# Kernel optimization log

Measured on AMD Instinct MI355X. Metric: run time of the kernel, lower is better.

Reference implementation:

```python
import jax, jax.numpy as jnp
import numpy as np
from math import sqrt

ALPHA = 1.0
EPS = 1e-8


def setup_inputs() -> dict:
    key = jax.random.key(0)
    k1, k2, k3 = jax.random.split(key, 3)
    B, L, S, H, E = 4, 2048, 2048, 8, 64
    queries = jax.random.normal(k1, (B, L, H, E), dtype=jnp.float32)
    keys = jax.random.normal(k2, (B, S, H, E), dtype=jnp.float32)
    values = jax.random.normal(k3, (B, S, H, E), dtype=jnp.float32)
    return {"queries": queries, "keys": keys, "values": values}


def reference(queries, keys, values):
    B, L, H, E = queries.shape
    scale = 1.0 / sqrt(E)
    # [B,H,L,S] dot-product scores
    dot_product = jnp.einsum('blhe,bshe->bhls', queries, keys)
    # squared norms: [B,H,L,1] and [B,H,1,S]
    queries_norm2 = jnp.sum(queries * queries, axis=-1).transpose(0, 2, 1)[..., None]
    keys_norm2 = jnp.sum(keys * keys, axis=-1).transpose(0, 2, 1)[..., None, :]
    # wedge (exterior product) norm: |q|^2|k|^2 - (q.k)^2, clamped at 0
    wedge_norm2 = jax.nn.relu(queries_norm2 * keys_norm2 - dot_product * dot_product)
    wedge_norm = jnp.sqrt(wedge_norm2 + EPS)
    scores = ((1.0 - ALPHA) * dot_product + ALPHA * wedge_norm) * scale
    A = jax.nn.softmax(scores, axis=-1)  # dropout p=0 (eval)
    V = jnp.einsum('bhls,bshd->blhd', A, values)
    return V, jnp.mean(jnp.abs(scores))
```

## Files before the change

### kernel.cpp

```cpp
#include <hip/hip_runtime.h>
#include <hip/hip_bf16.h>


#define B_ 4
#define L_ 2048
#define S_ 2048
#define H_ 8
#define E_ 64
#define EPS_ 1e-8f
#define SC2_ 0.18033688011112042f
#define LN2_ 0.6931471805599453f
#define LDP 72
#define ROWSTR (H_ * E_)

#define K_OFF 0
#define V_OFF 8388608
#define KN_OFF 16777216
#define SS_OFF 17039360
#define WS_NEED 17039364

typedef __attribute__((ext_vector_type(8))) short bf16x8;
typedef __attribute__((ext_vector_type(4))) short bf16x4v;
typedef __attribute__((ext_vector_type(4))) float f32x4;

static __device__ __forceinline__ short f2bf_rne(float x) {
  union { float f; unsigned u; } v; v.f = x;
  unsigned r = (v.u + 0x7FFF + ((v.u >> 16) & 1)) >> 16;
  return (short)(unsigned short)r;
}
static __device__ __forceinline__ float bf2f(short h) {
  union { unsigned u; float f; } v; v.u = ((unsigned)(unsigned short)h) << 16;
  return v.f;
}
static __device__ __forceinline__ float fast_sqrt(float x) {
  float r; asm("v_sqrt_f32 %0, %1" : "=v"(r) : "v"(x)); return r;
}
static __device__ __forceinline__ float fast_exp2(float x) {
  float r; asm("v_exp_f32 %0, %1" : "=v"(r) : "v"(x)); return r;
}
static __device__ __forceinline__ void gload16(const void* g, void* l) {
  __builtin_amdgcn_global_load_lds((const __attribute__((address_space(1))) void*)g,
                                   (__attribute__((address_space(3))) void*)l, 16, 0, 0);
}

__global__ void prep_k(const float* __restrict__ K, short* __restrict__ Kg,
                       float* __restrict__ kn2g) {
  const int tid = threadIdx.x;
  const int bidx = blockIdx.x;
  const int st = bidx & 31;
  const int bh = bidx >> 5;
  const int b = bh >> 3, h = bh & 7;
  const size_t src_base = (size_t)b * (L_ * ROWSTR) + (size_t)(st * 64) * ROWSTR + (size_t)h * E_;
  short* dst = Kg + (size_t)bidx * 4096;

  const int s = tid >> 2;
  float part = 0.f;
#pragma unroll
  for (int q = 0; q < 2; ++q) {
    const int ci = 2 * tid + q;
    const int ch = ci & 7;
    const int esrc = (ch ^ (s & 7)) * 8;
    const float* sp = K + src_base + (size_t)s * ROWSTR + esrc;
    const float4 a = *reinterpret_cast<const float4*>(sp);
    const float4 c4 = *reinterpret_cast<const float4*>(sp + 4);
    part += a.x*a.x + a.y*a.y + a.z*a.z + a.w*a.w
          + c4.x*c4.x + c4.y*c4.y + c4.z*c4.z + c4.w*c4.w;
    bf16x8 o;
    o[0]=f2bf_rne(a.x); o[1]=f2bf_rne(a.y); o[2]=f2bf_rne(a.z); o[3]=f2bf_rne(a.w);
    o[4]=f2bf_rne(c4.x); o[5]=f2bf_rne(c4.y); o[6]=f2bf_rne(c4.z); o[7]=f2bf_rne(c4.w);
    *reinterpret_cast<bf16x8*>(dst + s * 64 + ch * 8) = o;
  }
  part += __shfl_xor(part, 1);
  part += __shfl_xor(part, 2);
  if ((tid & 3) == 0) kn2g[(size_t)bidx * 64 + s] = part;
}

__global__ void prep_v(const float* __restrict__ V, short* __restrict__ Vg) {
  __shared__ __align__(16) short TT[64][72];
  const int tid = threadIdx.x;
  const int bidx = blockIdx.x;
  const int st = bidx & 31;
  const int bh = bidx >> 5;
  const int b = bh >> 3, h = bh & 7;
  const size_t src_base = (size_t)b * (L_ * ROWSTR) + (size_t)(st * 64) * ROWSTR + (size_t)h * E_;
  short* dst = Vg + (size_t)bidx * 4096;

  const int s = tid >> 2;
  const int e0 = (tid & 3) * 16;
  const float* sp = V + src_base + (size_t)s * ROWSTR + e0;
#pragma unroll
  for (int q = 0; q < 4; ++q) {
    const float4 a = *reinterpret_cast<const float4*>(sp + q * 4);
    TT[e0 + q*4 + 0][s] = f2bf_rne(a.x);
    TT[e0 + q*4 + 1][s] = f2bf_rne(a.y);
    TT[e0 + q*4 + 2][s] = f2bf_rne(a.z);
    TT[e0 + q*4 + 3][s] = f2bf_rne(a.w);
  }
  __syncthreads();
  const int e = s;
#pragma unroll
  for (int q = 0; q < 2; ++q) {
    const int ci = 2 * tid + q;
    const int ch = ci & 7;
    const int ssrc = (ch ^ (e & 7)) * 8;
    const bf16x8 v = *reinterpret_cast<const bf16x8*>(&TT[e][ssrc]);
    *reinterpret_cast<bf16x8*>(dst + e * 64 + ch * 8) = v;
  }
}

__launch_bounds__(256, 2)
__global__ void geom_attn(const float* __restrict__ Q,
                          const short* __restrict__ Kg,
                          const short* __restrict__ Vg,
                          const float* __restrict__ kn2g,
                          float* __restrict__ out,
                          float* __restrict__ ssum_g) {
  __shared__ __align__(16) short Kl[2][4096];
  __shared__ __align__(16) short Vl[2][4096];
  __shared__ __align__(16) short Plds[4][16 * LDP];

  const int tid = threadIdx.x;
  const int lane = tid & 63;
  const int w = tid >> 6;
  const int g = lane >> 4;
  const int c = lane & 15;
  const int cx = c & 7;

  const int vbk = ((blockIdx.x & 7) << 7) + (blockIdx.x >> 3);
  const int qt = vbk & 31;
  const int bh = vbk >> 5;
  const int b = bh >> 3, h = bh & 7;
  const int q0 = qt * 64;

  const size_t qbase = (size_t)b * (L_ * ROWSTR) + (size_t)h * E_;

  bf16x8 qa[2];
  float qn2row[4];
  {
    const int qrow = q0 + w * 16 + c;
    const float* qp = Q + qbase + (size_t)qrow * ROWSTR;
    float qs = 0.f;
#pragma unroll
    for (int ch = 0; ch < 2; ++ch) {
      const float4 a = *reinterpret_cast<const float4*>(qp + ch * 32 + g * 8);
      const float4 b4 = *reinterpret_cast<const float4*>(qp + ch * 32 + g * 8 + 4);
      qa[ch][0]=f2bf_rne(a.x); qa[ch][1]=f2bf_rne(a.y); qa[ch][2]=f2bf_rne(a.z); qa[ch][3]=f2bf_rne(a.w);
      qa[ch][4]=f2bf_rne(b4.x); qa[ch][5]=f2bf_rne(b4.y); qa[ch][6]=f2bf_rne(b4.z); qa[ch][7]=f2bf_rne(b4.w);
      qs += a.x*a.x + a.y*a.y + a.z*a.z + a.w*a.w
          + b4.x*b4.x + b4.y*b4.y + b4.z*b4.z + b4.w*b4.w;
    }
    qs += __shfl_xor(qs, 16);
    qs += __shfl_xor(qs, 32);
#pragma unroll
    for (int i = 0; i < 4; ++i) qn2row[i] = __shfl(qs, g * 4 + i);
  }

  float lsum[4] = {0.f, 0.f, 0.f, 0.f};
  f32x4 o[4];
#pragma unroll
  for (int dt = 0; dt < 4; ++dt) o[dt] = (f32x4){0.f, 0.f, 0.f, 0.f};
  float ssum = 0.f;

  const char* Ksrc = (const char*)(Kg + (size_t)(bh * 32) * 4096);
  const char* Vsrc = (const char*)(Vg + (size_t)(bh * 32) * 4096);
  const float* knb = kn2g + (size_t)(bh * 32) * 64;

  const int wb = w * 2048;

  gload16(Ksrc + wb + lane * 16,        (char*)&Kl[0][0] + wb);
  gload16(Ksrc + wb + 1024 + lane * 16, (char*)&Kl[0][0] + wb + 1024);
  gload16(Vsrc + wb + lane * 16,        (char*)&Vl[0][0] + wb);
  gload16(Vsrc + wb + 1024 + lane * 16, (char*)&Vl[0][0] + wb + 1024);

  for (int kt = 0; kt < 32; ++kt) {
    const int cb = kt & 1;
    __syncthreads();

    if (kt + 1 < 32) {
      const char* ks2 = Ksrc + (size_t)(kt + 1) * 8192;
      const char* vs2 = Vsrc + (size_t)(kt + 1) * 8192;
      gload16(ks2 + wb + lane * 16,        (char*)&Kl[cb ^ 1][0] + wb);
      gload16(ks2 + wb + 1024 + lane * 16, (char*)&Kl[cb ^ 1][0] + wb + 1024);
      gload16(vs2 + wb + lane * 16,        (char*)&Vl[cb ^ 1][0] + wb);
      gload16(vs2 + wb + 1024 + lane * 16, (char*)&Vl[cb ^ 1][0] + wb + 1024);
    }

    float kn_r[4];
#pragma unroll
    for (int sub = 0; sub < 4; ++sub) kn_r[sub] = knb[kt * 64 + sub * 16 + c];

#pragma unroll
    for (int sub = 0; sub < 4; ++sub) {
      const int s = sub * 16 + c;
      f32x4 acc = (f32x4){0.f, 0.f, 0.f, 0.f};
#pragma unroll
      for (int ch = 0; ch < 2; ++ch) {
        const int idx = s * 64 + (((ch * 4 + g) ^ cx) << 3);
        const bf16x8 bh8 = *reinterpret_cast<const bf16x8*>(&Kl[cb][idx]);
        acc = __builtin_amdgcn_mfma_f32_16x16x32_bf16(qa[ch], bh8, acc, 0, 0, 0);
      }
#pragma unroll
      for (int i = 0; i < 4; ++i) {
        const float dot = acc[i];
        const float w2 = fmaxf(fmaf(-dot, dot, qn2row[i] * kn_r[sub]), EPS_);
        const float s2 = SC2_ * fast_sqrt(w2);
        ssum += s2;
        const float p = fast_exp2(s2);
        union { float f; unsigned u; } pu; pu.f = p;
        union { unsigned u; float f; } pt; pt.u = pu.u & 0xffff0000u;
        lsum[i] += pt.f;
        Plds[w][(g * 4 + i) * LDP + s] = (short)(unsigned short)(pu.u >> 16);
      }
    }

#pragma unroll
    for (int ks = 0; ks < 2; ++ks) {
      const bf16x8 pa = *reinterpret_cast<const bf16x8*>(&Plds[w][c * LDP + ks * 32 + g * 8]);
#pragma unroll
      for (int dt = 0; dt < 4; ++dt) {
        const int er = dt * 16 + c;
        const int idx = er * 64 + (((ks * 4 + g) ^ cx) << 3);
        const bf16x8 vb8 = *reinterpret_cast<const bf16x8*>(&Vl[cb][idx]);
        o[dt] = __builtin_amdgcn_mfma_f32_16x16x32_bf16(pa, vb8, o[dt], 0, 0, 0);
      }
    }
  }

#pragma unroll
  for (int m = 1; m < 16; m <<= 1)
#pragma unroll
    for (int i = 0; i < 4; ++i) lsum[i] += __shfl_xor(lsum[i], m);

#pragma unroll
  for (int i = 0; i < 4; ++i) {
    const float inv = 1.0f / lsum[i];
    const int qrow = q0 + w * 16 + g * 4 + i;
    float* op = out + (size_t)b * (L_ * ROWSTR) + (size_t)qrow * ROWSTR + (size_t)h * E_;
#pragma unroll
    for (int dt = 0; dt < 4; ++dt)
      op[dt * 16 + c] = o[dt][i] * inv;
  }

#pragma unroll
  for (int m = 1; m < 64; m <<= 1) ssum += __shfl_xor(ssum, m);
  if (lane == 0) atomicAdd(ssum_g, ssum);
}

__global__ void geom_fin(const float* __restrict__ ws, float* __restrict__ out) {
  out[(size_t)B_ * L_ * H_ * E_] = ws[0] * (LN2_ / 134217728.0f);
}

__launch_bounds__(256, 2)
__global__ void geom_attn_v1(const float* __restrict__ Q, const float* __restrict__ K,
                             const float* __restrict__ V, float* __restrict__ out,
                             float* __restrict__ score_sum) {
  __shared__ __align__(16) short Khi[64 * LDP];
  __shared__ __align__(16) short Klo[64 * LDP];
  __shared__ __align__(16) short Vt[64 * LDP];
  __shared__ __align__(16) short Plds[4][16 * LDP];
  __shared__ float kn2[64];
  __shared__ float qn2[64];

  const int tid = threadIdx.x;
  const int lane = tid & 63;
  const int w = tid >> 6;
  const int g = lane >> 4;
  const int c = lane & 15;
  const int bidx = blockIdx.x;
  const int qt = bidx & 31;
  const int h = (bidx >> 5) & 7;
  const int b = bidx >> 8;
  const int q0 = qt * 64;
  const size_t bh_base = (size_t)b * L_ * ROWSTR + (size_t)h * E_;

  bf16x8 qhi[2], qlo[2];
  {
    const int qrow = q0 + w * 16 + c;
    const float* qp = Q + bh_base + (size_t)qrow * ROWSTR;
    float qs = 0.f;
#pragma unroll
    for (int ch = 0; ch < 2; ++ch) {
      const float4 a = *reinterpret_cast<const float4*>(qp + ch * 32 + g * 8);
      const float4 bq = *reinterpret_cast<const float4*>(qp + ch * 32 + g * 8 + 4);
      const float xs[8] = {a.x,a.y,a.z,a.w,bq.x,bq.y,bq.z,bq.w};
#pragma unroll
      for (int j = 0; j < 8; ++j) {
        const float x = xs[j];
        qs += x * x;
        const short hs = f2bf_rne(x);
        qhi[ch][j] = hs;
        qlo[ch][j] = f2bf_rne(x - bf2f(hs));
      }
    }
    qs += __shfl_xor(qs, 16);
    qs += __shfl_xor(qs, 32);
    if (lane < 16) qn2[w * 16 + c] = qs;
  }
  __syncthreads();
  float qn2row[4];
#pragma unroll
  for (int i = 0; i < 4; ++i) qn2row[i] = qn2[w * 16 + g * 4 + i];

  float m_i[4] = {0,0,0,0}, lsum[4] = {0,0,0,0};
  f32x4 o[4];
#pragma unroll
  for (int dt = 0; dt < 4; ++dt) o[dt] = (f32x4){0,0,0,0};
  float ssum = 0.f;

  for (int kt = 0; kt < S_ / 64; ++kt) {
    __syncthreads();
    {
      const int r0 = tid >> 4, c4 = tid & 15;
      const size_t kbase = bh_base + (size_t)(kt * 64) * ROWSTR + c4 * 4;
      float part[4];
#pragma unroll
      for (int i = 0; i < 4; ++i) {
        const int r = r0 + 16 * i;
        const float4 kv = *reinterpret_cast<const float4*>(K + kbase + (size_t)r * ROWSTR);
        part[i] = kv.x*kv.x + kv.y*kv.y + kv.z*kv.z + kv.w*kv.w;
        const short h0 = f2bf_rne(kv.x), h1 = f2bf_rne(kv.y), h2 = f2bf_rne(kv.z), h3 = f2bf_rne(kv.w);
        bf16x4v hv = {h0, h1, h2, h3};
        *reinterpret_cast<bf16x4v*>(&Khi[r * LDP + c4 * 4]) = hv;
        bf16x4v lv = {f2bf_rne(kv.x - bf2f(h0)), f2bf_rne(kv.y - bf2f(h1)),
                      f2bf_rne(kv.z - bf2f(h2)), f2bf_rne(kv.w - bf2f(h3))};
        *reinterpret_cast<bf16x4v*>(&Klo[r * LDP + c4 * 4]) = lv;
        const float4 vv = *reinterpret_cast<const float4*>(V + kbase + (size_t)r * ROWSTR);
        Vt[(c4 * 4 + 0) * LDP + r] = f2bf_rne(vv.x);
        Vt[(c4 * 4 + 1) * LDP + r] = f2bf_rne(vv.y);
        Vt[(c4 * 4 + 2) * LDP + r] = f2bf_rne(vv.z);
        Vt[(c4 * 4 + 3) * LDP + r] = f2bf_rne(vv.w);
      }
#pragma unroll
      for (int m = 1; m < 16; m <<= 1)
#pragma unroll
        for (int i = 0; i < 4; ++i) part[i] += __shfl_xor(part[i], m);
      if (c4 < 4) kn2[r0 + 16 * c4] = part[c4];
    }
    __syncthreads();

    float sv[4][4];
    float tm[4] = {0,0,0,0};
#pragma unroll
    for (int sub = 0; sub < 4; ++sub) {
      const int s = sub * 16 + c;
      f32x4 acc = (f32x4){0,0,0,0};
#pragma unroll
      for (int ch = 0; ch < 2; ++ch) {
        const int e = ch * 32 + g * 8;
        const bf16x8 bh8 = *reinterpret_cast<const bf16x8*>(&Khi[s * LDP + e]);
        const bf16x8 bl8 = *reinterpret_cast<const bf16x8*>(&Klo[s * LDP + e]);
        acc = __builtin_amdgcn_mfma_f32_16x16x32_bf16(qhi[ch], bh8, acc, 0, 0, 0);
        acc = __builtin_amdgcn_mfma_f32_16x16x32_bf16(qlo[ch], bh8, acc, 0, 0, 0);
        acc = __builtin_amdgcn_mfma_f32_16x16x32_bf16(qhi[ch], bl8, acc, 0, 0, 0);
      }
      const float kn = kn2[s];
#pragma unroll
      for (int i = 0; i < 4; ++i) {
        const float dot = acc[i];
        float w2 = fmaxf(qn2row[i] * kn - dot * dot, 0.f) + EPS_;
        const float sc = 0.125f * sqrtf(w2);
        sv[sub][i] = sc;
        tm[i] = fmaxf(tm[i], sc);
        ssum += sc;
      }
    }
#pragma unroll
    for (int m = 1; m < 16; m <<= 1)
#pragma unroll
      for (int i = 0; i < 4; ++i) tm[i] = fmaxf(tm[i], __shfl_xor(tm[i], m));
    float r_[4];
#pragma unroll
    for (int i = 0; i < 4; ++i) {
      const float mn = fmaxf(m_i[i], tm[i]);
      r_[i] = __expf(m_i[i] - mn);
      m_i[i] = mn;
      lsum[i] *= r_[i];
    }
#pragma unroll
    for (int dt = 0; dt < 4; ++dt)
#pragma unroll
      for (int i = 0; i < 4; ++i) o[dt][i] *= r_[i];
#pragma unroll
    for (int sub = 0; sub < 4; ++sub) {
      const int s = sub * 16 + c;
#pragma unroll
      for (int i = 0; i < 4; ++i) {
        const float p = __expf(sv[sub][i] - m_i[i]);
        lsum[i] += p;
        Plds[w][(g * 4 + i) * LDP + s] = f2bf_rne(p);
      }
    }
    __syncthreads();
#pragma unroll
    for (int ks = 0; ks < 2; ++ks) {
      const bf16x8 pa = *reinterpret_cast<const bf16x8*>(&Plds[w][c * LDP + ks * 32 + g * 8]);
#pragma unroll
      for (int dt = 0; dt < 4; ++dt) {
        const bf16x8 vb8 = *reinterpret_cast<const bf16x8*>(&Vt[(dt * 16 + c) * LDP + ks * 32 + g * 8]);
        o[dt] = __builtin_amdgcn_mfma_f32_16x16x32_bf16(pa, vb8, o[dt], 0, 0, 0);
      }
    }
  }
#pragma unroll
  for (int m = 1; m < 16; m <<= 1)
#pragma unroll
    for (int i = 0; i < 4; ++i) lsum[i] += __shfl_xor(lsum[i], m);
#pragma unroll
  for (int i = 0; i < 4; ++i) {
    const float inv = 1.0f / lsum[i];
    const int qrow = q0 + w * 16 + g * 4 + i;
    float* op = out + (size_t)b * L_ * ROWSTR + (size_t)qrow * ROWSTR + (size_t)h * E_;
#pragma unroll
    for (int dt = 0; dt < 4; ++dt) op[dt * 16 + c] = o[dt][i] * inv;
  }
#pragma unroll
  for (int m = 1; m < 64; m <<= 1) ssum += __shfl_xor(ssum, m);
  if (lane == 0) atomicAdd(score_sum, ssum);
}

__global__ void geom_fin_v1(const float* __restrict__ ws, float* __restrict__ out) {
  out[(size_t)B_ * L_ * H_ * E_] = ws[0] * (1.0f / 134217728.0f);
}

extern "C" void kernel_launch(void* const* d_in, const int* in_sizes, int n_in,
                              void* d_out, int out_size, void* d_ws, size_t ws_size,
                              hipStream_t stream) {
  const float* Q = (const float*)d_in[0];
  const float* K = (const float*)d_in[1];
  const float* V = (const float*)d_in[2];
  float* out = (float*)d_out;

  if (ws_size >= (size_t)WS_NEED) {
    short* Kg = (short*)((char*)d_ws + K_OFF);
    short* Vg = (short*)((char*)d_ws + V_OFF);
    float* kn2g = (float*)((char*)d_ws + KN_OFF);
    float* ss = (float*)((char*)d_ws + SS_OFF);
    hipMemsetAsync(ss, 0, sizeof(float), stream);
    prep_k<<<dim3(1024), dim3(256), 0, stream>>>(K, Kg, kn2g);
    prep_v<<<dim3(1024), dim3(256), 0, stream>>>(V, Vg);
    geom_attn<<<dim3(1024), dim3(256), 0, stream>>>(Q, Kg, Vg, kn2g, out, ss);
    geom_fin<<<dim3(1), dim3(1), 0, stream>>>(ss, out);
  } else {
    float* ss = (float*)d_ws;
    hipMemsetAsync(ss, 0, sizeof(float), stream);
    geom_attn_v1<<<dim3(1024), dim3(256), 0, stream>>>(Q, K, V, out, ss);
    geom_fin_v1<<<dim3(1), dim3(1), 0, stream>>>(ss, out);
  }
}
```

Baseline: 209.5 us.

## Merge K/V prep kernels, single-buffer V, raise occupancy, prefetch key norms

Fuses the separate K and V preparation kernels into one launch and switches to packed bf16 conversion intrinsics. In the attention kernel, V is now single-buffered: it is loaded at the start of each tile and waited on with a manual vmcnt plus barrier before the PV MFMAs. This frees LDS so launch bounds can rise from 2 to 4 blocks per CU. Key norms are also prefetched one tile ahead. The cost is that V load latency is exposed inside each iteration instead of being hidden by double-buffering, and there is an extra barrier per tile.

```diff
diff --git a/kernel.cpp b/kernel.cpp
--- a/kernel.cpp
+++ b/kernel.cpp
@@ -23,6 +23,13 @@
 typedef __attribute__((ext_vector_type(4))) short bf16x4v;
 typedef __attribute__((ext_vector_type(4))) float f32x4;
 
+union bfr8 { bf16x8 v; unsigned u[4]; };
+
+static __device__ __forceinline__ unsigned pk2(float lo, float hi) {
+  union { __hip_bfloat162 h2; unsigned u; } cv;
+  cv.h2 = __float22bfloat162_rn(float2{lo, hi});
+  return cv.u;
+}
 static __device__ __forceinline__ short f2bf_rne(float x) {
   union { float f; unsigned u; } v; v.f = x;
   unsigned r = (v.u + 0x7FFF + ((v.u >> 16) & 1)) >> 16;
@@ -43,72 +50,77 @@
                                    (__attribute__((address_space(3))) void*)l, 16, 0, 0);
 }
 
-__global__ void prep_k(const float* __restrict__ K, short* __restrict__ Kg,
-                       float* __restrict__ kn2g) {
+__global__ void prep_kv(const float* __restrict__ K, const float* __restrict__ V,
+                        short* __restrict__ Kg, short* __restrict__ Vg,
+                        float* __restrict__ kn2g) {
+  __shared__ __align__(16) short TT[64 * 80];
   const int tid = threadIdx.x;
-  const int bidx = blockIdx.x;
+  const int raw = blockIdx.x;
+  const bool isK = raw < 1024;
+  const int bidx = isK ? raw : raw - 1024;
   const int st = bidx & 31;
   const int bh = bidx >> 5;
   const int b = bh >> 3, h = bh & 7;
   const size_t src_base = (size_t)b * (L_ * ROWSTR) + (size_t)(st * 64) * ROWSTR + (size_t)h * E_;
-  short* dst = Kg + (size_t)bidx * 4096;
-
-  const int s = tid >> 2;
-  float part = 0.f;
-#pragma unroll
-  for (int q = 0; q < 2; ++q) {
-    const int ci = 2 * tid + q;
-    const int ch = ci & 7;
-    const int esrc = (ch ^ (s & 7)) * 8;
-    const float* sp = K + src_base + (size_t)s * ROWSTR + esrc;
-    const float4 a = *reinterpret_cast<const float4*>(sp);
-    const float4 c4 = *reinterpret_cast<const float4*>(sp + 4);
-    part += a.x*a.x + a.y*a.y + a.z*a.z + a.w*a.w
-          + c4.x*c4.x + c4.y*c4.y + c4.z*c4.z + c4.w*c4.w;
-    bf16x8 o;
-    o[0]=f2bf_rne(a.x); o[1]=f2bf_rne(a.y); o[2]=f2bf_rne(a.z); o[3]=f2bf_rne(a.w);
-    o[4]=f2bf_rne(c4.x); o[5]=f2bf_rne(c4.y); o[6]=f2bf_rne(c4.z); o[7]=f2bf_rne(c4.w);
-    *reinterpret_cast<bf16x8*>(dst + s * 64 + ch * 8) = o;
-  }
-  part += __shfl_xor(part, 1);
-  part += __shfl_xor(part, 2);
-  if ((tid & 3) == 0) kn2g[(size_t)bidx * 64 + s] = part;
-}
-
-__global__ void prep_v(const float* __restrict__ V, short* __restrict__ Vg) {
-  __shared__ __align__(16) short TT[64][72];
-  const int tid = threadIdx.x;
-  const int bidx = blockIdx.x;
-  const int st = bidx & 31;
-  const int bh = bidx >> 5;
-  const int b = bh >> 3, h = bh & 7;
-  const size_t src_base = (size_t)b * (L_ * ROWSTR) + (size_t)(st * 64) * ROWSTR + (size_t)h * E_;
-  short* dst = Vg + (size_t)bidx * 4096;
-
-  const int s = tid >> 2;
-  const int e0 = (tid & 3) * 16;
-  const float* sp = V + src_base + (size_t)s * ROWSTR + e0;
-#pragma unroll
-  for (int q = 0; q < 4; ++q) {
-    const float4 a = *reinterpret_cast<const float4*>(sp + q * 4);
-    TT[e0 + q*4 + 0][s] = f2bf_rne(a.x);
-    TT[e0 + q*4 + 1][s] = f2bf_rne(a.y);
-    TT[e0 + q*4 + 2][s] = f2bf_rne(a.z);
-    TT[e0 + q*4 + 3][s] = f2bf_rne(a.w);
-  }
-  __syncthreads();
-  const int e = s;
-#pragma unroll
-  for (int q = 0; q < 2; ++q) {
-    const int ci = 2 * tid + q;
-    const int ch = ci & 7;
-    const int ssrc = (ch ^ (e & 7)) * 8;
-    const bf16x8 v = *reinterpret_cast<const bf16x8*>(&TT[e][ssrc]);
-    *reinterpret_cast<bf16x8*>(dst + e * 64 + ch * 8) = v;
-  }
-}
-
-__launch_bounds__(256, 2)
+
+  if (isK) {
+    short* dst = Kg + (size_t)bidx * 4096;
+    const int s = tid >> 2;
+    float part = 0.f;
+#pragma unroll
+    for (int q = 0; q < 2; ++q) {
+      const int ch = (2 * tid + q) & 7;
+      const int esrc = (ch ^ (s & 7)) * 8;
+      const float* sp = K + src_base + (size_t)s * ROWSTR + esrc;
+      const float4 a = *reinterpret_cast<const float4*>(sp);
+      const float4 c4 = *reinterpret_cast<const float4*>(sp + 4);
+      part += a.x*a.x + a.y*a.y + a.z*a.z + a.w*a.w
+            + c4.x*c4.x + c4.y*c4.y + c4.z*c4.z + c4.w*c4.w;
+      bfr8 o;
+      o.u[0] = pk2(a.x, a.y);  o.u[1] = pk2(a.z, a.w);
+      o.u[2] = pk2(c4.x, c4.y); o.u[3] = pk2(c4.z, c4.w);
+      *reinterpret_cast<bf16x8*>(dst + s * 64 + ch * 8) = o.v;
+    }
+    part += __shfl_xor(part, 1);
+    part += __shfl_xor(part, 2);
+    if ((tid & 3) == 0) kn2g[(size_t)bidx * 64 + s] = part;
+  } else {
+    short* dst = Vg + (size_t)bidx * 4096;
+    {
+      const int s = tid >> 2;
+      const int e0 = (tid & 3) * 16;
+      const float* sp = V + src_base + (size_t)s * ROWSTR + e0;
+      const float4 a0 = *reinterpret_cast<const float4*>(sp);
+      const float4 a1 = *reinterpret_cast<const float4*>(sp + 4);
+      const float4 a2 = *reinterpret_cast<const float4*>(sp + 8);
+      const float4 a3 = *reinterpret_cast<const float4*>(sp + 12);
+      bfr8 t0, t1;
+      t0.u[0] = pk2(a0.x, a0.y); t0.u[1] = pk2(a0.z, a0.w);
+      t0.u[2] = pk2(a1.x, a1.y); t0.u[3] = pk2(a1.z, a1.w);
+      t1.u[0] = pk2(a2.x, a2.y); t1.u[1] = pk2(a2.z, a2.w);
+      t1.u[2] = pk2(a3.x, a3.y); t1.u[3] = pk2(a3.z, a3.w);
+      *reinterpret_cast<bf16x8*>(&TT[s * 80 + e0]) = t0.v;
+      *reinterpret_cast<bf16x8*>(&TT[s * 80 + e0 + 8]) = t1.v;
+    }
+    __syncthreads();
+    const int e = tid >> 2;
+#pragma unroll
+    for (int q = 0; q < 2; ++q) {
+      const int ch = (2 * tid + q) & 7;
+      const int s0 = (ch ^ (e & 7)) * 8;
+      bfr8 o;
+#pragma unroll
+      for (int j = 0; j < 4; ++j) {
+        const unsigned lo = (unsigned short)TT[(s0 + 2 * j) * 80 + e];
+        const unsigned hi = (unsigned short)TT[(s0 + 2 * j + 1) * 80 + e];
+        o.u[j] = lo | (hi << 16);
+      }
+      *reinterpret_cast<bf16x8*>(dst + e * 64 + ch * 8) = o.v;
+    }
+  }
+}
+
+__launch_bounds__(256, 4)
 __global__ void geom_attn(const float* __restrict__ Q,
                           const short* __restrict__ Kg,
                           const short* __restrict__ Vg,
@@ -116,7 +128,7 @@
                           float* __restrict__ out,
                           float* __restrict__ ssum_g) {
   __shared__ __align__(16) short Kl[2][4096];
-  __shared__ __align__(16) short Vl[2][4096];
+  __shared__ __align__(16) short Vl[4096];
   __shared__ __align__(16) short Plds[4][16 * LDP];
 
   const int tid = threadIdx.x;
@@ -134,7 +146,7 @@
 
   const size_t qbase = (size_t)b * (L_ * ROWSTR) + (size_t)h * E_;
 
-  bf16x8 qa[2];
+  bfr8 qa[2];
   float qn2row[4];
   {
     const int qrow = q0 + w * 16 + c;
@@ -144,8 +156,8 @@
     for (int ch = 0; ch < 2; ++ch) {
       const float4 a = *reinterpret_cast<const float4*>(qp + ch * 32 + g * 8);
       const float4 b4 = *reinterpret_cast<const float4*>(qp + ch * 32 + g * 8 + 4);
-      qa[ch][0]=f2bf_rne(a.x); qa[ch][1]=f2bf_rne(a.y); qa[ch][2]=f2bf_rne(a.z); qa[ch][3]=f2bf_rne(a.w);
-      qa[ch][4]=f2bf_rne(b4.x); qa[ch][5]=f2bf_rne(b4.y); qa[ch][6]=f2bf_rne(b4.z); qa[ch][7]=f2bf_rne(b4.w);
+      qa[ch].u[0] = pk2(a.x, a.y);  qa[ch].u[1] = pk2(a.z, a.w);
+      qa[ch].u[2] = pk2(b4.x, b4.y); qa[ch].u[3] = pk2(b4.z, b4.w);
       qs += a.x*a.x + a.y*a.y + a.z*a.z + a.w*a.w
           + b4.x*b4.x + b4.y*b4.y + b4.z*b4.z + b4.w*b4.w;
     }
@@ -167,27 +179,27 @@
 
   const int wb = w * 2048;
 
+  float kn_cur[4], kn_next[4];
+#pragma unroll
+  for (int sub = 0; sub < 4; ++sub) kn_cur[sub] = knb[sub * 16 + c];
+
   gload16(Ksrc + wb + lane * 16,        (char*)&Kl[0][0] + wb);
   gload16(Ksrc + wb + 1024 + lane * 16, (char*)&Kl[0][0] + wb + 1024);
-  gload16(Vsrc + wb + lane * 16,        (char*)&Vl[0][0] + wb);
-  gload16(Vsrc + wb + 1024 + lane * 16, (char*)&Vl[0][0] + wb + 1024);
 
   for (int kt = 0; kt < 32; ++kt) {
     const int cb = kt & 1;
+    const int nx = (kt + 1) & 31;
     __syncthreads();
 
-    if (kt + 1 < 32) {
-      const char* ks2 = Ksrc + (size_t)(kt + 1) * 8192;
-      const char* vs2 = Vsrc + (size_t)(kt + 1) * 8192;
-      gload16(ks2 + wb + lane * 16,        (char*)&Kl[cb ^ 1][0] + wb);
-      gload16(ks2 + wb + 1024 + lane * 16, (char*)&Kl[cb ^ 1][0] + wb + 1024);
-      gload16(vs2 + wb + lane * 16,        (char*)&Vl[cb ^ 1][0] + wb);
-      gload16(vs2 + wb + 1024 + lane * 16, (char*)&Vl[cb ^ 1][0] + wb + 1024);
-    }
-
-    float kn_r[4];
-#pragma unroll
-    for (int sub = 0; sub < 4; ++sub) kn_r[sub] = knb[kt * 64 + sub * 16 + c];
+#pragma unroll
+    for (int sub = 0; sub < 4; ++sub) kn_next[sub] = knb[nx * 64 + sub * 16 + c];
+    __builtin_amdgcn_sched_barrier(0);
+    const char* vs = Vsrc + (size_t)kt * 8192;
+    gload16(vs + wb + lane * 16,        (char*)&Vl[0] + wb);
+    gload16(vs + wb + 1024 + lane * 16, (char*)&Vl[0] + wb + 1024);
+    const char* ks = Ksrc + (size_t)nx * 8192;
+    gload16(ks + wb + lane * 16,        (char*)&Kl[cb ^ 1][0] + wb);
+    gload16(ks + wb + 1024 + lane * 16, (char*)&Kl[cb ^ 1][0] + wb + 1024);
 
 #pragma unroll
     for (int sub = 0; sub < 4; ++sub) {
@@ -197,12 +209,12 @@
       for (int ch = 0; ch < 2; ++ch) {
         const int idx = s * 64 + (((ch * 4 + g) ^ cx) << 3);
         const bf16x8 bh8 = *reinterpret_cast<const bf16x8*>(&Kl[cb][idx]);
-        acc = __builtin_amdgcn_mfma_f32_16x16x32_bf16(qa[ch], bh8, acc, 0, 0, 0);
+        acc = __builtin_amdgcn_mfma_f32_16x16x32_bf16(qa[ch].v, bh8, acc, 0, 0, 0);
       }
 #pragma unroll
       for (int i = 0; i < 4; ++i) {
         const float dot = acc[i];
-        const float w2 = fmaxf(fmaf(-dot, dot, qn2row[i] * kn_r[sub]), EPS_);
+        const float w2 = fmaxf(fmaf(-dot, dot, qn2row[i] * kn_cur[sub]), EPS_);
         const float s2 = SC2_ * fast_sqrt(w2);
         ssum += s2;
         const float p = fast_exp2(s2);
@@ -213,17 +225,21 @@
       }
     }
 
-#pragma unroll
-    for (int ks = 0; ks < 2; ++ks) {
-      const bf16x8 pa = *reinterpret_cast<const bf16x8*>(&Plds[w][c * LDP + ks * 32 + g * 8]);
+    asm volatile("s_waitcnt vmcnt(2)\n\ts_barrier" ::: "memory");
+
+#pragma unroll
+    for (int ks2 = 0; ks2 < 2; ++ks2) {
+      const bf16x8 pa = *reinterpret_cast<const bf16x8*>(&Plds[w][c * LDP + ks2 * 32 + g * 8]);
 #pragma unroll
       for (int dt = 0; dt < 4; ++dt) {
         const int er = dt * 16 + c;
-        const int idx = er * 64 + (((ks * 4 + g) ^ cx) << 3);
-        const bf16x8 vb8 = *reinterpret_cast<const bf16x8*>(&Vl[cb][idx]);
+        const int idx = er * 64 + (((ks2 * 4 + g) ^ cx) << 3);
+        const bf16x8 vb8 = *reinterpret_cast<const bf16x8*>(&Vl[idx]);
         o[dt] = __builtin_amdgcn_mfma_f32_16x16x32_bf16(pa, vb8, o[dt], 0, 0, 0);
       }
     }
+#pragma unroll
+    for (int sub = 0; sub < 4; ++sub) kn_cur[sub] = kn_next[sub];
   }
 
 #pragma unroll
@@ -436,8 +452,7 @@
     float* kn2g = (float*)((char*)d_ws + KN_OFF);
     float* ss = (float*)((char*)d_ws + SS_OFF);
     hipMemsetAsync(ss, 0, sizeof(float), stream);
-    prep_k<<<dim3(1024), dim3(256), 0, stream>>>(K, Kg, kn2g);
-    prep_v<<<dim3(1024), dim3(256), 0, stream>>>(V, Vg);
+    prep_kv<<<dim3(2048), dim3(256), 0, stream>>>(K, V, Kg, Vg, kn2g);
     geom_attn<<<dim3(1024), dim3(256), 0, stream>>>(Q, Kg, Vg, kn2g, out, ss);
     geom_fin<<<dim3(1), dim3(1), 0, stream>>>(ss, out);
   } else {
```

New measurement: 193.8 us. -7.5%, faster.
